# Kernel optimization log

Measured on AMD Instinct MI355X. Metric: run time of the kernel, lower is better.

## Reference

```python
import jax, jax.numpy as jnp
import numpy as np

B, T, E, H = 8, 2048, 128, 4
FACTOR = 3  # autocorr_factor


def setup_inputs() -> dict:
    key = jax.random.key(0)
    ks = jax.random.split(key, 9)
    s = 0.05
    return {
        "hidden_states": jax.random.normal(ks[0], (B, T, E), jnp.float32),
        "wq": jax.random.normal(ks[1], (E, E, H), jnp.float32) * s,
        "bq": jax.random.normal(ks[2], (E, H), jnp.float32) * s,
        "wk": jax.random.normal(ks[3], (E, E, H), jnp.float32) * s,
        "bk": jax.random.normal(ks[4], (E, H), jnp.float32) * s,
        "wv": jax.random.normal(ks[5], (E, E, H), jnp.float32) * s,
        "bv": jax.random.normal(ks[6], (E, H), jnp.float32) * s,
        "wo": jax.random.normal(ks[7], (E, H, E), jnp.float32) * s,
        "bo": jax.random.normal(ks[8], (E,), jnp.float32) * s,
    }


def reference(hidden_states, wq, bq, wk, bk, wv, bv, wo, bo):
    # Inference path (training=None) of AutoCorrelation.call
    bsize, seq_len, _ = hidden_states.shape
    q = jnp.einsum('btj,juh->btuh', hidden_states, wq) + bq  # [B,T,E,H]
    k = jnp.einsum('btj,juh->btuh', hidden_states, wk) + bk
    v = jnp.einsum('btj,juh->btuh', hidden_states, wv) + bv

    # FFT cross-correlation over time axis
    qf = jnp.fft.rfft(q.transpose(0, 2, 3, 1), n=seq_len, axis=-1)  # [B,E,H,F]
    kf = jnp.fft.rfft(k.transpose(0, 2, 3, 1), n=seq_len, axis=-1)
    ac = jnp.fft.irfft(qf * jnp.conj(kf), n=seq_len, axis=-1)       # [B,E,H,T]
    ac = ac.transpose(0, 3, 1, 2)                                   # [B,T,E,H]

    ac_mean = ac.mean(axis=-1)                                      # [B,T,E]
    top_k = int(FACTOR * np.log(float(seq_len)))

    # top-k delays per (batch, channel)
    vals, idx = jax.lax.top_k(ac_mean.transpose(0, 2, 1), top_k)    # [B,E,K]
    w = jax.nn.softmax(vals, axis=-1)  # == Softmax(axis=-2) on [B,K,E]

    # NOTE: in the source, `delays_agg +=` is dedented outside the top_k loop,
    # so only the LAST iteration (i = top_k-1) contributes. Replicated faithfully.
    delay = idx[:, :, top_k - 1]   # [B,E] int
    wgt = w[:, :, top_k - 1]       # [B,E]

    # gather over doubled values == circular roll by -delay per (b, channel)
    t_idx = (jnp.arange(seq_len)[None, :, None] + delay[:, None, :]) % seq_len  # [B,T,E]
    rolled = jnp.take_along_axis(v, t_idx[..., None], axis=1)       # [B,T,E,H]
    agg = rolled * wgt[:, None, :, None]                            # [B,T,E,H]

    return jnp.einsum('btjh,jhf->btf', agg, wo) + bo                # [B,T,E]
```

## Files before the change

kernel.cpp:

```cpp
#include <hip/hip_runtime.h>
#include <math.h>

#define TSEQ 2048
#define BB 8
#define EE 128
#define HH 4
#define UHN 512
#define KTOP 22
#define BT (BB*TSEQ)
#define PITCH 76

typedef _Float16 f16;
typedef f16 f16x2 __attribute__((ext_vector_type(2)));
typedef f16 f16x4 __attribute__((ext_vector_type(4)));
typedef f16 f16x8 __attribute__((ext_vector_type(8)));
typedef float f32x4 __attribute__((ext_vector_type(4)));

__device__ __forceinline__ float2 cmul(float2 a, float2 b) {
  return make_float2(a.x*b.x - a.y*b.y, a.x*b.y + a.y*b.x);
}
__device__ __forceinline__ float2 cadd(float2 a, float2 b) {
  return make_float2(a.x + b.x, a.y + b.y);
}
__device__ __forceinline__ float2 csub(float2 a, float2 b) {
  return make_float2(a.x - b.x, a.y - b.y);
}

__device__ __forceinline__ f16x8 ld_frag(const f16* p) {
  f16x4 lo = *(const f16x4*)(p);
  f16x4 hi = *(const f16x4*)(p + 16);
  return __builtin_shufflevector(lo, hi, 0, 1, 2, 3, 4, 5, 6, 7);
}

__global__ __launch_bounds__(256, 2)
void proj_mfma(const float* __restrict__ hs,
               const float* __restrict__ wq, const float* __restrict__ bq,
               const float* __restrict__ wk, const float* __restrict__ bk,
               const float* __restrict__ wv, const float* __restrict__ bv,
               float* __restrict__ q_t, float* __restrict__ k_t, float* __restrict__ v_t)
{
  __shared__ f16 Ah[128*PITCH];
  __shared__ f16 Al[128*PITCH];
  __shared__ f16 Bh[128*PITCH];
  __shared__ f16 Bl[128*PITCH];

  const float* W; const float* bias; float* outp;
  if (blockIdx.z == 0)      { W = wq; bias = bq; outp = q_t; }
  else if (blockIdx.z == 1) { W = wk; bias = bk; outp = k_t; }
  else                      { W = wv; bias = bv; outp = v_t; }

  const int tid  = threadIdx.x;
  const int lane = tid & 63, wid = tid >> 6;
  const int wm = wid >> 1, wn = wid & 1;
  const int ln15 = lane & 15, g = lane >> 4;
  const int uh0 = blockIdx.x * 128;
  const int bt0 = blockIdx.y * 128;

  f32x4 acc[4][4] = {};

  for (int kc = 0; kc < 2; ++kc) {
    const int k0 = kc * 64;
    __syncthreads();
#pragma unroll
    for (int r = 0; r < 16; ++r) {
      int idx = tid + 256*r;
      int u = idx & 127, kp = idx >> 7;
      float w0 = W[(size_t)(k0 + 2*kp    )*UHN + uh0 + u];
      float w1 = W[(size_t)(k0 + 2*kp + 1)*UHN + uh0 + u];
      f16 h0 = (f16)w0, h1 = (f16)w1;
      f16 l0 = (f16)(w0 - (float)h0), l1 = (f16)(w1 - (float)h1);
      *(f16x2*)&Ah[u*PITCH + 2*kp] = (f16x2){h0, h1};
      *(f16x2*)&Al[u*PITCH + 2*kp] = (f16x2){l0, l1};
    }
#pragma unroll
    for (int r = 0; r < 8; ++r) {
      int idx4 = tid + 256*r;
      int tl = idx4 >> 4, kq = idx4 & 15;
      float4 hv = *(const float4*)&hs[(size_t)(bt0 + tl)*EE + k0 + 4*kq];
      f16 h0 = (f16)hv.x, h1 = (f16)hv.y, h2 = (f16)hv.z, h3 = (f16)hv.w;
      *(f16x4*)&Bh[tl*PITCH + 4*kq] = (f16x4){h0, h1, h2, h3};
      *(f16x4*)&Bl[tl*PITCH + 4*kq] =
        (f16x4){(f16)(hv.x - (float)h0), (f16)(hv.y - (float)h1),
                (f16)(hv.z - (float)h2), (f16)(hv.w - (float)h3)};
    }
    __syncthreads();
#pragma unroll
    for (int ks = 0; ks < 2; ++ks) {
      const int kb = ks*32 + 4*g;
      f16x8 a_h[4], a_l[4], b_h[4], b_l[4];
#pragma unroll
      for (int mf = 0; mf < 4; ++mf) {
        int off = (wm*64 + mf*16 + ln15)*PITCH + kb;
        a_h[mf] = ld_frag(&Ah[off]);
        a_l[mf] = ld_frag(&Al[off]);
      }
#pragma unroll
      for (int nf = 0; nf < 4; ++nf) {
        int off = (wn*64 + nf*16 + ln15)*PITCH + kb;
        b_h[nf] = ld_frag(&Bh[off]);
        b_l[nf] = ld_frag(&Bl[off]);
      }
#pragma unroll
      for (int mf = 0; mf < 4; ++mf)
#pragma unroll
        for (int nf = 0; nf < 4; ++nf) {
          acc[mf][nf] = __builtin_amdgcn_mfma_f32_16x16x32_f16(a_h[mf], b_h[nf], acc[mf][nf], 0, 0, 0);
          acc[mf][nf] = __builtin_amdgcn_mfma_f32_16x16x32_f16(a_h[mf], b_l[nf], acc[mf][nf], 0, 0, 0);
          acc[mf][nf] = __builtin_amdgcn_mfma_f32_16x16x32_f16(a_l[mf], b_h[nf], acc[mf][nf], 0, 0, 0);
        }
    }
  }

  const int b = bt0 >> 11, tb = bt0 & (TSEQ - 1);
#pragma unroll
  for (int mf = 0; mf < 4; ++mf) {
    int uhb = uh0 + wm*64 + mf*16 + g*4;
    f32x4 bias4 = *(const f32x4*)&bias[uhb];
#pragma unroll
    for (int r = 0; r < 4; ++r) {
      size_t rowbase = ((size_t)(b*UHN + uhb + r))*TSEQ + tb;
#pragma unroll
      for (int nf = 0; nf < 4; ++nf) {
        int t = wn*64 + nf*16 + ln15;
        outp[rowbase + t] = acc[mf][nf][r] + bias4[r];
      }
    }
  }
}

#define ZPAD(g) ((g) + ((g) >> 5))

template<int SGN>
__device__ __forceinline__ float2 addim(float2 a, float2 b) {
  return (SGN < 0) ? make_float2(a.x + b.y, a.y - b.x)
                   : make_float2(a.x - b.y, a.y + b.x);
}
template<int SGN>
__device__ __forceinline__ float2 subim(float2 a, float2 b) {
  return (SGN < 0) ? make_float2(a.x - b.y, a.y + b.x)
                   : make_float2(a.x + b.y, a.y - b.x);
}

template<int SGN>
__device__ __forceinline__ void dft8(const float2* u, float2* y) {
  const float r2 = 0.70710678118654752440f;
  float2 a0 = cadd(u[0], u[4]), a1 = cadd(u[1], u[5]);
  float2 a2 = cadd(u[2], u[6]), a3 = cadd(u[3], u[7]);
  float2 b0 = csub(u[0], u[4]), b1 = csub(u[1], u[5]);
  float2 b2 = csub(u[2], u[6]), b3 = csub(u[3], u[7]);
  float2 t1 = (SGN < 0) ? make_float2(r2*(b1.x + b1.y), r2*(b1.y - b1.x))
                        : make_float2(r2*(b1.x - b1.y), r2*(b1.y + b1.x));
  float2 t2 = (SGN < 0) ? make_float2(b2.y, -b2.x) : make_float2(-b2.y, b2.x);
  float2 e  = (SGN < 0) ? make_float2(r2*(b3.x + b3.y), r2*(b3.y - b3.x))
                        : make_float2(r2*(b3.x - b3.y), r2*(b3.y + b3.x));
  float2 t3 = (SGN < 0) ? make_float2(e.y, -e.x) : make_float2(-e.y, e.x);
  {
    float2 c0 = cadd(a0, a2), c1 = csub(a0, a2);
    float2 c2 = cadd(a1, a3), c3 = csub(a1, a3);
    y[0] = cadd(c0, c2); y[4] = csub(c0, c2);
    y[2] = addim<SGN>(c1, c3); y[6] = subim<SGN>(c1, c3);
  }
  {
    float2 c0 = cadd(b0, t2), c1 = csub(b0, t2);
    float2 c2 = cadd(t1, t3), c3 = csub(t1, t3);
    y[1] = cadd(c0, c2); y[5] = csub(c0, c2);
    y[3] = addim<SGN>(c1, c3); y[7] = subim<SGN>(c1, c3);
  }
}

__device__ __forceinline__ void fwd_radix8(float2* Z, float2 w1, int base, int eighth) {
  float2 u[8];
#pragma unroll
  for (int t = 0; t < 8; ++t) u[t] = Z[ZPAD(base + eighth*t)];
  float2 y[8];
  dft8<-1>(u, y);
  Z[ZPAD(base)] = y[0];
  float2 w = w1;
  Z[ZPAD(base + eighth)] = cmul(y[1], w);
#pragma unroll
  for (int s = 2; s < 8; ++s) {
    w = cmul(w, w1);
    Z[ZPAD(base + eighth*s)] = cmul(y[s], w);
  }
}

__device__ __forceinline__ void inv_radix8(float2* Z, float2 w1c, int base, int eighth) {
  float2 u[8];
#pragma unroll
  for (int t = 0; t < 8; ++t) u[t] = Z[ZPAD(base + eighth*t)];
  u[1] = cmul(u[1], w1c);
  float2 w = w1c;
#pragma unroll
  for (int t = 2; t < 8; ++t) {
    w = cmul(w, w1c);
    u[t] = cmul(u[t], w);
  }
  float2 y[8];
  dft8<1>(u, y);
#pragma unroll
  for (int s = 0; s < 8; ++s) Z[ZPAD(base + eighth*s)] = y[s];
}

template<int SGN>
__device__ __forceinline__ void radix4_stage(float2* Z, int base) {
  float2 v0 = Z[ZPAD(base)], v1 = Z[ZPAD(base+1)];
  float2 v2 = Z[ZPAD(base+2)], v3 = Z[ZPAD(base+3)];
  float2 c0 = cadd(v0, v2), c1 = csub(v0, v2);
  float2 c2 = cadd(v1, v3), c3 = csub(v1, v3);
  Z[ZPAD(base)]   = cadd(c0, c2);
  Z[ZPAD(base+1)] = addim<SGN>(c1, c3);
  Z[ZPAD(base+2)] = csub(c0, c2);
  Z[ZPAD(base+3)] = subim<SGN>(c1, c3);
}

__global__ __launch_bounds__(256)
void fftcorr_kernel(const float* __restrict__ q_t, const float* __restrict__ k_t,
                    float* __restrict__ ac)
{
  __shared__ float2 Z[2112];
  __shared__ float2 twl[292];

  const int tid = threadIdx.x;
  const int bu  = blockIdx.x;

  for (int idx = tid; idx < 292; idx += 256) {
    float ang;
    if (idx < 256)      ang = -6.2831853071795864769f * (float)idx / 2048.0f;
    else if (idx < 288) ang = -6.2831853071795864769f * (float)(idx - 256) / 256.0f;
    else                ang = -6.2831853071795864769f * (float)(idx - 288) / 32.0f;
    float s, c;
    sincosf(ang, &s, &c);
    twl[idx] = make_float2(c, s);
  }
  const float2* tw1 = twl;
  const float2* tw2 = twl + 256;
  const float2* tw3 = twl + 288;

  int pp[8];
#pragma unroll
  for (int r = 0; r < 8; ++r) {
    int p = tid + (r << 8);
    int f = ((p >> 8) & 7) | (((p >> 5) & 7) << 3) | (((p >> 2) & 7) << 6) | ((p & 3) << 9);
    int nf = (2048 - f) & 2047;
    pp[r] = ((nf & 7) << 8) | (((nf >> 3) & 7) << 5) | (((nf >> 6) & 7) << 2) | ((nf >> 9) & 3);
  }
  float2 sreg[8] = {};
  __syncthreads();

  for (int h = 0; h < HH; ++h) {
    const float* qp = q_t + ((size_t)bu*HH + h)*TSEQ;
    const float* kp = k_t + ((size_t)bu*HH + h)*TSEQ;
    {
      float2 u[8];
#pragma unroll
      for (int t = 0; t < 8; ++t)
        u[t] = make_float2(qp[tid + 256*t], kp[tid + 256*t]);
      float2 y[8];
      dft8<-1>(u, y);
      float2 w1 = tw1[tid];
      Z[ZPAD(tid)] = y[0];
      float2 w = w1;
      Z[ZPAD(tid + 256)] = cmul(y[1], w);
#pragma unroll
      for (int s = 2; s < 8; ++s) {
        w = cmul(w, w1);
        Z[ZPAD(tid + 256*s)] = cmul(y[s], w);
      }
    }
    __syncthreads();
    fwd_radix8(Z, tw2[tid & 31], ((tid >> 5) << 8) + (tid & 31), 32);
    __syncthreads();
    fwd_radix8(Z, tw3[tid & 3], ((tid >> 2) << 5) + (tid & 3), 4);
    __syncthreads();
    radix4_stage<-1>(Z, 4*tid);
    radix4_stage<-1>(Z, 4*(tid + 256));
    __syncthreads();
#pragma unroll
    for (int r = 0; r < 8; ++r) {
      int p = tid + (r << 8);
      float2 A  = Z[ZPAD(p)];
      float2 Zp = Z[ZPAD(pp[r])];
      sreg[r].x += 0.5f  * (Zp.x*A.y + Zp.y*A.x);
      sreg[r].y += 0.25f * ((A.x*A.x + A.y*A.y) - (Zp.x*Zp.x + Zp.y*Zp.y));
    }
    __syncthreads();
  }

#pragma unroll
  for (int r = 0; r < 8; ++r) Z[ZPAD(tid + (r << 8))] = sreg[r];
  __syncthreads();
  radix4_stage<1>(Z, 4*tid);
  radix4_stage<1>(Z, 4*(tid + 256));
  __syncthreads();
  { float2 w = tw3[tid & 3]; w.y = -w.y;
    inv_radix8(Z, w, ((tid >> 2) << 5) + (tid & 3), 4); }
  __syncthreads();
  { float2 w = tw2[tid & 31]; w.y = -w.y;
    inv_radix8(Z, w, ((tid >> 5) << 8) + (tid & 31), 32); }
  __syncthreads();
  {
    float2 u[8];
#pragma unroll
    for (int t = 0; t < 8; ++t) u[t] = Z[ZPAD(tid + 256*t)];
    float2 w1c = tw1[tid]; w1c.y = -w1c.y;
    u[1] = cmul(u[1], w1c);
    float2 w = w1c;
#pragma unroll
    for (int t = 2; t < 8; ++t) {
      w = cmul(w, w1c);
      u[t] = cmul(u[t], w);
    }
    float2 y[8];
    dft8<1>(u, y);
    const float scale = 1.0f / (float)(TSEQ * HH);
#pragma unroll
    for (int s = 0; s < 8; ++s)
      ac[(size_t)bu*TSEQ + tid + 256*s] = y[s].x * scale;
  }
}

__global__ __launch_bounds__(256)
void topk_kernel(const float* __restrict__ ac, int* __restrict__ delay,
                 float* __restrict__ wgt)
{
  __shared__ float v[TSEQ];
  __shared__ float rv[4];
  __shared__ int   ri[4];

  const int tid = threadIdx.x;
  const int bu  = blockIdx.x;

#pragma unroll
  for (int r = 0; r < 8; ++r) {
    int i = tid + 256*r;
    v[i] = ac[(size_t)bu*TSEQ + i];
  }

  float m0 = 0.f, ssum = 0.f;
  for (int it = 0; it < KTOP; ++it) {
    __syncthreads();
    float best = -3.4e38f; int bi = 0;
#pragma unroll
    for (int r = 0; r < 8; ++r) {
      int i = tid + 256*r;
      float x = v[i];
      if (x > best) { best = x; bi = i; }
    }
#pragma unroll
    for (int off = 32; off > 0; off >>= 1) {
      float ob = __shfl_down(best, off);
      int   oi = __shfl_down(bi, off);
      if (ob > best || (ob == best && oi < bi)) { best = ob; bi = oi; }
    }
    if ((tid & 63) == 0) { rv[tid >> 6] = best; ri[tid >> 6] = bi; }
    __syncthreads();
    if (tid == 0) {
      float gb = rv[0]; int gi = ri[0];
      for (int w2 = 1; w2 < 4; ++w2)
        if (rv[w2] > gb || (rv[w2] == gb && ri[w2] < gi)) { gb = rv[w2]; gi = ri[w2]; }
      v[gi] = -3.4e38f;
      if (it == 0) m0 = gb;
      ssum += expf(gb - m0);
      if (it == KTOP - 1) {
        delay[bu] = gi;
        wgt[bu]   = expf(gb - m0) / ssum;
      }
    }
  }
}

__global__ __launch_bounds__(256)
void out_mfma(const float* __restrict__ v_t, const int* __restrict__ delay,
              const float* __restrict__ wgt, const float* __restrict__ wo,
              const float* __restrict__ bo, float* __restrict__ out)
{
  __shared__ f16 Af[64*PITCH];
  __shared__ f16 Bf[64*PITCH];
  __shared__ int   dly[EE];
  __shared__ float wg[EE];

  const int tid  = threadIdx.x;
  const int lane = tid & 63, wid = tid >> 6;
  const int wm = wid >> 1, wn = wid & 1;
  const int ln15 = lane & 15, g = lane >> 4;
  const int t0g = blockIdx.x * 64;
  const int f0  = blockIdx.y * 64;
  const int b = t0g >> 11, t0 = t0g & (TSEQ - 1);

  if (tid < EE) { dly[tid] = delay[b*EE + tid]; wg[tid] = wgt[b*EE + tid]; }

  f32x4 acc[2][2] = {};

  for (int c = 0; c < 8; ++c) {
    const int uh0 = c * 64;
    __syncthreads();
#pragma unroll
    for (int r = 0; r < 16; ++r) {
      int idx = tid + 256*r;
      int tl = idx & 63, ul = idx >> 6;
      int u = (uh0 + ul) >> 2;
      float x = v_t[((size_t)(b*UHN + uh0 + ul))*TSEQ + ((t0 + tl + dly[u]) & (TSEQ-1))]
                * wg[u];
      Af[tl*PITCH + ul] = (f16)x;
    }
#pragma unroll
    for (int r = 0; r < 16; ++r) {
      int idx = tid + 256*r;
      int fl = idx & 63, ul = idx >> 6;
      Bf[fl*PITCH + ul] = (f16)wo[(size_t)(uh0 + ul)*EE + f0 + fl];
    }
    __syncthreads();
#pragma unroll
    for (int ks = 0; ks < 2; ++ks) {
      const int kb = ks*32 + 4*g;
      f16x8 av[2], bv[2];
#pragma unroll
      for (int mf = 0; mf < 2; ++mf)
        av[mf] = ld_frag(&Af[(wm*32 + mf*16 + ln15)*PITCH + kb]);
#pragma unroll
      for (int nf = 0; nf < 2; ++nf)
        bv[nf] = ld_frag(&Bf[(wn*32 + nf*16 + ln15)*PITCH + kb]);
#pragma unroll
      for (int mf = 0; mf < 2; ++mf)
#pragma unroll
        for (int nf = 0; nf < 2; ++nf)
          acc[mf][nf] = __builtin_amdgcn_mfma_f32_16x16x32_f16(av[mf], bv[nf], acc[mf][nf], 0, 0, 0);
    }
  }

#pragma unroll
  for (int mf = 0; mf < 2; ++mf)
#pragma unroll
    for (int r = 0; r < 4; ++r) {
      int bt = t0g + wm*32 + mf*16 + g*4 + r;
#pragma unroll
      for (int nf = 0; nf < 2; ++nf) {
        int f = f0 + wn*32 + nf*16 + ln15;
        out[(size_t)bt*EE + f] = acc[mf][nf][r] + bo[f];
      }
    }
}

extern "C" void kernel_launch(void* const* d_in, const int* in_sizes, int n_in,
                              void* d_out, int out_size, void* d_ws, size_t ws_size,
                              hipStream_t stream) {
  (void)in_sizes; (void)n_in; (void)out_size; (void)ws_size;
  const float* hs = (const float*)d_in[0];
  const float* wq = (const float*)d_in[1];
  const float* bq = (const float*)d_in[2];
  const float* wk = (const float*)d_in[3];
  const float* bk = (const float*)d_in[4];
  const float* wv = (const float*)d_in[5];
  const float* bv = (const float*)d_in[6];
  const float* wo = (const float*)d_in[7];
  const float* bo = (const float*)d_in[8];
  float* out = (float*)d_out;

  const size_t NQ = (size_t)BB * UHN * TSEQ;
  float* q_t = (float*)d_ws;
  float* k_t = q_t + NQ;
  float* v_t = k_t + NQ;
  float* ac  = v_t + NQ;
  int*   delay = (int*)(ac + (size_t)BB*EE*TSEQ);
  float* wgt   = (float*)(delay + BB*EE);

  proj_mfma<<<dim3(4, 128, 3), 256, 0, stream>>>(hs, wq, bq, wk, bk, wv, bv,
                                                 q_t, k_t, v_t);
  fftcorr_kernel<<<dim3(1024), 256, 0, stream>>>(q_t, k_t, ac);
  topk_kernel<<<dim3(1024), 256, 0, stream>>>(ac, delay, wgt);
  out_mfma<<<dim3(256, 2), 256, 0, stream>>>(v_t, delay, wgt, wo, bo, out);
}
```

Before: 116.6 us.

## Precompute fp16 split operands, fuse FFT with top-k, store V in fp16

Adds a prep kernel that converts hidden states and weights once into hi/lo fp16 split form, with weights transposed. The projection GEMM then loads fp16 tiles with wide vector loads instead of converting fp32 on the fly in every block. The FFT correlation kernel now runs top-k selection in shared memory, so the autocorrelation array is no longer written to and reread from global memory. V is stored in fp16 and wo is pre-transposed, which halves V traffic in the output GEMM at some precision cost and adds one extra launch.

```diff
diff --git a/kernel.cpp b/kernel.cpp
--- a/kernel.cpp
+++ b/kernel.cpp
@@ -8,7 +8,8 @@
 #define UHN 512
 #define KTOP 22
 #define BT (BB*TSEQ)
-#define PITCH 76
+#define APITCH 40
+#define OPITCH 76
 
 typedef _Float16 f16;
 typedef f16 f16x2 __attribute__((ext_vector_type(2)));
@@ -32,22 +33,83 @@
   return __builtin_shufflevector(lo, hi, 0, 1, 2, 3, 4, 5, 6, 7);
 }
 
-__global__ __launch_bounds__(256, 2)
-void proj_mfma(const float* __restrict__ hs,
-               const float* __restrict__ wq, const float* __restrict__ bq,
-               const float* __restrict__ wk, const float* __restrict__ bk,
-               const float* __restrict__ wv, const float* __restrict__ bv,
-               float* __restrict__ q_t, float* __restrict__ k_t, float* __restrict__ v_t)
+__global__ __launch_bounds__(256)
+void prep_kernel(const float* __restrict__ hs,
+                 const float* __restrict__ wq, const float* __restrict__ wk,
+                 const float* __restrict__ wv, const float* __restrict__ wo,
+                 f16* __restrict__ hs_h, f16* __restrict__ hs_l,
+                 f16* __restrict__ Wt_h, f16* __restrict__ Wt_l,
+                 f16* __restrict__ wo_t)
 {
-  __shared__ f16 Ah[128*PITCH];
-  __shared__ f16 Al[128*PITCH];
-  __shared__ f16 Bh[128*PITCH];
-  __shared__ f16 Bl[128*PITCH];
-
-  const float* W; const float* bias; float* outp;
-  if (blockIdx.z == 0)      { W = wq; bias = bq; outp = q_t; }
-  else if (blockIdx.z == 1) { W = wk; bias = bk; outp = k_t; }
-  else                      { W = wv; bias = bv; outp = v_t; }
+  __shared__ float tile[64][65];
+  const int bx = blockIdx.x, tid = threadIdx.x;
+
+  if (bx < 1024) {
+    size_t base = ((size_t)bx*256 + tid) * 8;
+    float4 a = *(const float4*)&hs[base];
+    float4 b = *(const float4*)&hs[base + 4];
+    float vf[8] = {a.x,a.y,a.z,a.w, b.x,b.y,b.z,b.w};
+    f16 h[8], l[8];
+#pragma unroll
+    for (int j = 0; j < 8; ++j) { h[j] = (f16)vf[j]; l[j] = (f16)(vf[j] - (float)h[j]); }
+    *(f16x8*)&hs_h[base] = (f16x8){h[0],h[1],h[2],h[3],h[4],h[5],h[6],h[7]};
+    *(f16x8*)&hs_l[base] = (f16x8){l[0],l[1],l[2],l[3],l[4],l[5],l[6],l[7]};
+  } else if (bx < 1072) {
+    int r = bx - 1024;
+    int z = r >> 4, rem = r & 15, kt = rem & 1, uht = rem >> 1;
+    const float* W = (z == 0) ? wq : (z == 1) ? wk : wv;
+#pragma unroll
+    for (int rr = 0; rr < 16; ++rr) {
+      int idx = tid + 256*rr;
+      int krow = idx >> 6, ucol = idx & 63;
+      tile[krow][ucol] = W[(size_t)(kt*64 + krow)*UHN + uht*64 + ucol];
+    }
+    __syncthreads();
+#pragma unroll
+    for (int rr = 0; rr < 16; ++rr) {
+      int idx = tid + 256*rr;
+      int orow = idx >> 6, ocol = idx & 63;
+      float w = tile[ocol][orow];
+      f16 h = (f16)w;
+      size_t o = ((size_t)z*UHN + uht*64 + orow)*EE + kt*64 + ocol;
+      Wt_h[o] = h;
+      Wt_l[o] = (f16)(w - (float)h);
+    }
+  } else {
+    int r = bx - 1072;
+    int ft = r & 1, uht = r >> 1;
+#pragma unroll
+    for (int rr = 0; rr < 16; ++rr) {
+      int idx = tid + 256*rr;
+      int urow = idx >> 6, fcol = idx & 63;
+      tile[urow][fcol] = wo[(size_t)(uht*64 + urow)*EE + ft*64 + fcol];
+    }
+    __syncthreads();
+#pragma unroll
+    for (int rr = 0; rr < 16; ++rr) {
+      int idx = tid + 256*rr;
+      int orow = idx >> 6, ocol = idx & 63;
+      wo_t[(size_t)(ft*64 + orow)*UHN + uht*64 + ocol] = (f16)tile[ocol][orow];
+    }
+  }
+}
+
+__global__ __launch_bounds__(256, 3)
+void proj_mfma(const f16* __restrict__ hs_h, const f16* __restrict__ hs_l,
+               const f16* __restrict__ Wt_h, const f16* __restrict__ Wt_l,
+               const float* __restrict__ bq, const float* __restrict__ bk,
+               const float* __restrict__ bv,
+               float* __restrict__ q_t, float* __restrict__ k_t, f16* __restrict__ v_t)
+{
+  __shared__ f16 Ah[128*APITCH];
+  __shared__ f16 Al[128*APITCH];
+  __shared__ f16 Bh[128*APITCH];
+  __shared__ f16 Bl[128*APITCH];
+
+  const int z = blockIdx.z;
+  const float* bias = (z == 0) ? bq : (z == 1) ? bk : bv;
+  const f16* WH = Wt_h + (size_t)z*UHN*EE;
+  const f16* WL = Wt_l + (size_t)z*UHN*EE;
 
   const int tid  = threadIdx.x;
   const int lane = tid & 63, wid = tid >> 6;
@@ -58,71 +120,71 @@
 
   f32x4 acc[4][4] = {};
 
-  for (int kc = 0; kc < 2; ++kc) {
-    const int k0 = kc * 64;
-    __syncthreads();
-#pragma unroll
-    for (int r = 0; r < 16; ++r) {
+  for (int kc = 0; kc < 4; ++kc) {
+    const int k0 = kc * 32;
+    __syncthreads();
+#pragma unroll
+    for (int r = 0; r < 2; ++r) {
       int idx = tid + 256*r;
-      int u = idx & 127, kp = idx >> 7;
-      float w0 = W[(size_t)(k0 + 2*kp    )*UHN + uh0 + u];
-      float w1 = W[(size_t)(k0 + 2*kp + 1)*UHN + uh0 + u];
-      f16 h0 = (f16)w0, h1 = (f16)w1;
-      f16 l0 = (f16)(w0 - (float)h0), l1 = (f16)(w1 - (float)h1);
-      *(f16x2*)&Ah[u*PITCH + 2*kp] = (f16x2){h0, h1};
-      *(f16x2*)&Al[u*PITCH + 2*kp] = (f16x2){l0, l1};
-    }
-#pragma unroll
-    for (int r = 0; r < 8; ++r) {
-      int idx4 = tid + 256*r;
-      int tl = idx4 >> 4, kq = idx4 & 15;
-      float4 hv = *(const float4*)&hs[(size_t)(bt0 + tl)*EE + k0 + 4*kq];
-      f16 h0 = (f16)hv.x, h1 = (f16)hv.y, h2 = (f16)hv.z, h3 = (f16)hv.w;
-      *(f16x4*)&Bh[tl*PITCH + 4*kq] = (f16x4){h0, h1, h2, h3};
-      *(f16x4*)&Bl[tl*PITCH + 4*kq] =
-        (f16x4){(f16)(hv.x - (float)h0), (f16)(hv.y - (float)h1),
-                (f16)(hv.z - (float)h2), (f16)(hv.w - (float)h3)};
-    }
-    __syncthreads();
-#pragma unroll
-    for (int ks = 0; ks < 2; ++ks) {
-      const int kb = ks*32 + 4*g;
-      f16x8 a_h[4], a_l[4], b_h[4], b_l[4];
-#pragma unroll
-      for (int mf = 0; mf < 4; ++mf) {
-        int off = (wm*64 + mf*16 + ln15)*PITCH + kb;
-        a_h[mf] = ld_frag(&Ah[off]);
-        a_l[mf] = ld_frag(&Al[off]);
+      int row = idx >> 2, seg = (idx & 3) << 3;
+      size_t ga = (size_t)(uh0 + row)*EE + k0 + seg;
+      *(f16x8*)&Ah[row*APITCH + seg] = *(const f16x8*)&WH[ga];
+      *(f16x8*)&Al[row*APITCH + seg] = *(const f16x8*)&WL[ga];
+      size_t gb = (size_t)(bt0 + row)*EE + k0 + seg;
+      *(f16x8*)&Bh[row*APITCH + seg] = *(const f16x8*)&hs_h[gb];
+      *(f16x8*)&Bl[row*APITCH + seg] = *(const f16x8*)&hs_l[gb];
+    }
+    __syncthreads();
+    const int kb = 4*g;
+    f16x8 a_h[4], a_l[4], b_h[4], b_l[4];
+#pragma unroll
+    for (int mf = 0; mf < 4; ++mf) {
+      int off = (wm*64 + mf*16 + ln15)*APITCH + kb;
+      a_h[mf] = ld_frag(&Ah[off]);
+      a_l[mf] = ld_frag(&Al[off]);
+    }
+#pragma unroll
+    for (int nf = 0; nf < 4; ++nf) {
+      int off = (wn*64 + nf*16 + ln15)*APITCH + kb;
+      b_h[nf] = ld_frag(&Bh[off]);
+      b_l[nf] = ld_frag(&Bl[off]);
+    }
+#pragma unroll
+    for (int mf = 0; mf < 4; ++mf)
+#pragma unroll
+      for (int nf = 0; nf < 4; ++nf) {
+        acc[mf][nf] = __builtin_amdgcn_mfma_f32_16x16x32_f16(a_h[mf], b_h[nf], acc[mf][nf], 0, 0, 0);
+        acc[mf][nf] = __builtin_amdgcn_mfma_f32_16x16x32_f16(a_h[mf], b_l[nf], acc[mf][nf], 0, 0, 0);
+        acc[mf][nf] = __builtin_amdgcn_mfma_f32_16x16x32_f16(a_l[mf], b_h[nf], acc[mf][nf], 0, 0, 0);
       }
-#pragma unroll
-      for (int nf = 0; nf < 4; ++nf) {
-        int off = (wn*64 + nf*16 + ln15)*PITCH + kb;
-        b_h[nf] = ld_frag(&Bh[off]);
-        b_l[nf] = ld_frag(&Bl[off]);
+  }
+
+  const int b = bt0 >> 11, tb = bt0 & (TSEQ - 1);
+  if (z == 2) {
+#pragma unroll
+    for (int mf = 0; mf < 4; ++mf) {
+      int uhb = uh0 + wm*64 + mf*16 + g*4;
+      f32x4 bias4 = *(const f32x4*)&bias[uhb];
+#pragma unroll
+      for (int r = 0; r < 4; ++r) {
+        f16* vrow = v_t + ((size_t)(b*UHN + uhb + r))*TSEQ + tb;
+#pragma unroll
+        for (int nf = 0; nf < 4; ++nf)
+          vrow[wn*64 + nf*16 + ln15] = (f16)(acc[mf][nf][r] + bias4[r]);
       }
-#pragma unroll
-      for (int mf = 0; mf < 4; ++mf)
-#pragma unroll
-        for (int nf = 0; nf < 4; ++nf) {
-          acc[mf][nf] = __builtin_amdgcn_mfma_f32_16x16x32_f16(a_h[mf], b_h[nf], acc[mf][nf], 0, 0, 0);
-          acc[mf][nf] = __builtin_amdgcn_mfma_f32_16x16x32_f16(a_h[mf], b_l[nf], acc[mf][nf], 0, 0, 0);
-          acc[mf][nf] = __builtin_amdgcn_mfma_f32_16x16x32_f16(a_l[mf], b_h[nf], acc[mf][nf], 0, 0, 0);
-        }
-    }
-  }
-
-  const int b = bt0 >> 11, tb = bt0 & (TSEQ - 1);
-#pragma unroll
-  for (int mf = 0; mf < 4; ++mf) {
-    int uhb = uh0 + wm*64 + mf*16 + g*4;
-    f32x4 bias4 = *(const f32x4*)&bias[uhb];
-#pragma unroll
-    for (int r = 0; r < 4; ++r) {
-      size_t rowbase = ((size_t)(b*UHN + uhb + r))*TSEQ + tb;
-#pragma unroll
-      for (int nf = 0; nf < 4; ++nf) {
-        int t = wn*64 + nf*16 + ln15;
-        outp[rowbase + t] = acc[mf][nf][r] + bias4[r];
+    }
+  } else {
+    float* outp = (z == 0) ? q_t : k_t;
+#pragma unroll
+    for (int mf = 0; mf < 4; ++mf) {
+      int uhb = uh0 + wm*64 + mf*16 + g*4;
+      f32x4 bias4 = *(const f32x4*)&bias[uhb];
+#pragma unroll
+      for (int r = 0; r < 4; ++r) {
+        size_t rowbase = ((size_t)(b*UHN + uhb + r))*TSEQ + tb;
+#pragma unroll
+        for (int nf = 0; nf < 4; ++nf)
+          outp[rowbase + wn*64 + nf*16 + ln15] = acc[mf][nf][r] + bias4[r];
       }
     }
   }
@@ -214,11 +276,13 @@
 }
 
 __global__ __launch_bounds__(256)
-void fftcorr_kernel(const float* __restrict__ q_t, const float* __restrict__ k_t,
-                    float* __restrict__ ac)
+void fftcorr_topk(const float* __restrict__ q_t, const float* __restrict__ k_t,
+                  int* __restrict__ delay, float* __restrict__ wgt)
 {
   __shared__ float2 Z[2112];
   __shared__ float2 twl[292];
+  __shared__ float rv[4];
+  __shared__ int   ri[4];
 
   const int tid = threadIdx.x;
   const int bu  = blockIdx.x;
@@ -298,10 +362,13 @@
   { float2 w = tw2[tid & 31]; w.y = -w.y;
     inv_radix8(Z, w, ((tid >> 5) << 8) + (tid & 31), 32); }
   __syncthreads();
+
+  float* vbuf = (float*)Z;
   {
     float2 u[8];
 #pragma unroll
     for (int t = 0; t < 8; ++t) u[t] = Z[ZPAD(tid + 256*t)];
+    __syncthreads();
     float2 w1c = tw1[tid]; w1c.y = -w1c.y;
     u[1] = cmul(u[1], w1c);
     float2 w = w1c;
@@ -315,25 +382,7 @@
     const float scale = 1.0f / (float)(TSEQ * HH);
 #pragma unroll
     for (int s = 0; s < 8; ++s)
-      ac[(size_t)bu*TSEQ + tid + 256*s] = y[s].x * scale;
-  }
-}
-
-__global__ __launch_bounds__(256)
-void topk_kernel(const float* __restrict__ ac, int* __restrict__ delay,
-                 float* __restrict__ wgt)
-{
-  __shared__ float v[TSEQ];
-  __shared__ float rv[4];
-  __shared__ int   ri[4];
-
-  const int tid = threadIdx.x;
-  const int bu  = blockIdx.x;
-
-#pragma unroll
-  for (int r = 0; r < 8; ++r) {
-    int i = tid + 256*r;
-    v[i] = ac[(size_t)bu*TSEQ + i];
+      vbuf[tid + 256*s] = y[s].x * scale;
   }
 
   float m0 = 0.f, ssum = 0.f;
@@ -343,7 +392,7 @@
 #pragma unroll
     for (int r = 0; r < 8; ++r) {
       int i = tid + 256*r;
-      float x = v[i];
+      float x = vbuf[i];
       if (x > best) { best = x; bi = i; }
     }
 #pragma unroll
@@ -358,7 +407,7 @@
       float gb = rv[0]; int gi = ri[0];
       for (int w2 = 1; w2 < 4; ++w2)
         if (rv[w2] > gb || (rv[w2] == gb && ri[w2] < gi)) { gb = rv[w2]; gi = ri[w2]; }
-      v[gi] = -3.4e38f;
+      vbuf[gi] = -3.4e38f;
       if (it == 0) m0 = gb;
       ssum += expf(gb - m0);
       if (it == KTOP - 1) {
@@ -370,12 +419,12 @@
 }
 
 __global__ __launch_bounds__(256)
-void out_mfma(const float* __restrict__ v_t, const int* __restrict__ delay,
-              const float* __restrict__ wgt, const float* __restrict__ wo,
+void out_mfma(const f16* __restrict__ v_t, const int* __restrict__ delay,
+              const float* __restrict__ wgt, const f16* __restrict__ wo_t,
               const float* __restrict__ bo, float* __restrict__ out)
 {
-  __shared__ f16 Af[64*PITCH];
-  __shared__ f16 Bf[64*PITCH];
+  __shared__ f16 Af[64*OPITCH];
+  __shared__ f16 Bf[64*OPITCH];
   __shared__ int   dly[EE];
   __shared__ float wg[EE];
 
@@ -399,15 +448,17 @@
       int idx = tid + 256*r;
       int tl = idx & 63, ul = idx >> 6;
       int u = (uh0 + ul) >> 2;
-      float x = v_t[((size_t)(b*UHN + uh0 + ul))*TSEQ + ((t0 + tl + dly[u]) & (TSEQ-1))]
+      float x = (float)v_t[((size_t)(b*UHN + uh0 + ul))*TSEQ + ((t0 + tl + dly[u]) & (TSEQ-1))]
                 * wg[u];
-      Af[tl*PITCH + ul] = (f16)x;
-    }
-#pragma unroll
-    for (int r = 0; r < 16; ++r) {
+      Af[tl*OPITCH + ul] = (f16)x;
+    }
+#pragma unroll
+    for (int r = 0; r < 2; ++r) {
       int idx = tid + 256*r;
-      int fl = idx & 63, ul = idx >> 6;
-      Bf[fl*PITCH + ul] = (f16)wo[(size_t)(uh0 + ul)*EE + f0 + fl];
+      int fl = idx >> 3, seg = (idx & 7) << 3;
+      const f16* src = &wo_t[(size_t)(f0 + fl)*UHN + uh0 + seg];
+      *(f16x4*)&Bf[fl*OPITCH + seg]     = *(const f16x4*)(src);
+      *(f16x4*)&Bf[fl*OPITCH + seg + 4] = *(const f16x4*)(src + 4);
     }
     __syncthreads();
 #pragma unroll
@@ -416,10 +467,10 @@
       f16x8 av[2], bv[2];
 #pragma unroll
       for (int mf = 0; mf < 2; ++mf)
-        av[mf] = ld_frag(&Af[(wm*32 + mf*16 + ln15)*PITCH + kb]);
+        av[mf] = ld_frag(&Af[(wm*32 + mf*16 + ln15)*OPITCH + kb]);
 #pragma unroll
       for (int nf = 0; nf < 2; ++nf)
-        bv[nf] = ld_frag(&Bf[(wn*32 + nf*16 + ln15)*PITCH + kb]);
+        bv[nf] = ld_frag(&Bf[(wn*32 + nf*16 + ln15)*OPITCH + kb]);
 #pragma unroll
       for (int mf = 0; mf < 2; ++mf)
 #pragma unroll
@@ -456,17 +507,22 @@
   const float* bo = (const float*)d_in[8];
   float* out = (float*)d_out;
 
-  const size_t NQ = (size_t)BB * UHN * TSEQ;
-  float* q_t = (float*)d_ws;
-  float* k_t = q_t + NQ;
-  float* v_t = k_t + NQ;
-  float* ac  = v_t + NQ;
-  int*   delay = (int*)(ac + (size_t)BB*EE*TSEQ);
-  float* wgt   = (float*)(delay + BB*EE);
-
-  proj_mfma<<<dim3(4, 128, 3), 256, 0, stream>>>(hs, wq, bq, wk, bk, wv, bv,
-                                                 q_t, k_t, v_t);
-  fftcorr_kernel<<<dim3(1024), 256, 0, stream>>>(q_t, k_t, ac);
-  topk_kernel<<<dim3(1024), 256, 0, stream>>>(ac, delay, wgt);
-  out_mfma<<<dim3(256, 2), 256, 0, stream>>>(v_t, delay, wgt, wo, bo, out);
-}
+  char* p = (char*)d_ws;
+  float* q_t  = (float*)p;  p += (size_t)BB*UHN*TSEQ*4;
+  float* k_t  = (float*)p;  p += (size_t)BB*UHN*TSEQ*4;
+  f16*   v_t  = (f16*)p;    p += (size_t)BB*UHN*TSEQ*2;
+  f16*   hs_h = (f16*)p;    p += (size_t)BT*EE*2;
+  f16*   hs_l = (f16*)p;    p += (size_t)BT*EE*2;
+  f16*   Wt_h = (f16*)p;    p += (size_t)3*UHN*EE*2;
+  f16*   Wt_l = (f16*)p;    p += (size_t)3*UHN*EE*2;
+  f16*   wo_t = (f16*)p;    p += (size_t)EE*UHN*2;
+  int*   delay = (int*)p;   p += BB*EE*4;
+  float* wgt   = (float*)p;
+
+  prep_kernel<<<dim3(1088), 256, 0, stream>>>(hs, wq, wk, wv, wo,
+                                              hs_h, hs_l, Wt_h, Wt_l, wo_t);
+  proj_mfma<<<dim3(4, 128, 3), 256, 0, stream>>>(hs_h, hs_l, Wt_h, Wt_l,
+                                                 bq, bk, bv, q_t, k_t, v_t);
+  fftcorr_topk<<<dim3(1024), 256, 0, stream>>>(q_t, k_t, delay, wgt);
+  out_mfma<<<dim3(256, 2), 256, 0, stream>>>(v_t, delay, wgt, wo_t, bo, out);
+}
```

Result: slower. 119.7 us (+2.6%).
